# Kernel tuning notes

Hardware: AMD Instinct MI355X
Metric: run time of the kernel (lower is better)

Reference implementation:

```python
import jax, jax.numpy as jnp
import numpy as np

NUM_HEADS = 8
EPS = 1e-6


def setup_inputs() -> dict:
    key = jax.random.key(0)
    ks = jax.random.split(key, 6)
    B, C, H, W = 32, 512, 32, 32
    E = C
    scale = 1.0 / np.sqrt(E)
    x = jax.random.normal(ks[0], (B, C, H, W), dtype=jnp.float32)
    Wq = jax.random.normal(ks[1], (E, E), dtype=jnp.float32) * scale
    Wk = jax.random.normal(ks[2], (E, E), dtype=jnp.float32) * scale
    Wv = jax.random.normal(ks[3], (E, E), dtype=jnp.float32) * scale
    Wo = jax.random.normal(ks[4], (E, E), dtype=jnp.float32) * scale
    bo = jnp.zeros((E,), dtype=jnp.float32)
    return {"x": x, "Wq": Wq, "Wk": Wk, "Wv": Wv, "Wo": Wo, "bo": bo}


def reference(x, Wq, Wk, Wv, Wo, bo):
    B, C, H, W = x.shape
    S = H * W
    nh = NUM_HEADS
    hd = C // nh
    # (B, C, H, W) -> (B, S, C)
    t = x.reshape(B, C, S).transpose(0, 2, 1)
    # torch Linear: t @ W.T  (no bias for q/k/v)
    Q = (t @ Wq.T).reshape(B, S, nh, hd).transpose(0, 2, 1, 3)  # (B, nh, S, hd)
    K = (t @ Wk.T).reshape(B, S, nh, hd).transpose(0, 2, 1, 3)
    V = (t @ Wv.T).reshape(B, S, nh, hd).transpose(0, 2, 1, 3)
    phi_Q = jax.nn.elu(Q) + 1.0
    phi_K = jax.nn.elu(K) + 1.0
    # K^T V aggregation: (B, nh, hd, hd)
    KV = jnp.einsum('bhsd,bhse->bhde', phi_K, V)
    numerator = jnp.einsum('bhsd,bhde->bhse', phi_Q, KV)      # (B, nh, S, hd)
    # phi_K^T @ ones == sum over seq: (B, nh, hd)
    k_sum = jnp.sum(phi_K, axis=2)
    denominator = jnp.einsum('bhsd,bhd->bhs', phi_Q, k_sum)[..., None]  # (B, nh, S, 1)
    out = numerator / (denominator + EPS)
    out = out.transpose(0, 2, 1, 3).reshape(B, S, C)          # (B, S, C)
    out = out @ Wo.T + bo
    out = out.transpose(0, 2, 1).reshape(B, C, H, W)
    return out
```

## Files before the change

### kernel.cpp

```cpp
#include <hip/hip_runtime.h>
#include <hip/hip_bf16.h>

typedef __bf16 bf16;
typedef __bf16 bf16x2 __attribute__((ext_vector_type(2)));
typedef __bf16 bf16x4 __attribute__((ext_vector_type(4)));
typedef __bf16 bf16x8 __attribute__((ext_vector_type(8)));
typedef float  f32x4  __attribute__((ext_vector_type(4)));

#define MFMA16(a,b,c) __builtin_amdgcn_mfma_f32_16x16x32_bf16((a),(b),(c),0,0,0)

constexpr int Cn = 512;
constexpr int Sn = 1024;

__global__ __launch_bounds__(256) void k_cvt_w(const float* __restrict__ Wq,
                                               const float* __restrict__ Wk,
                                               const float* __restrict__ Wv,
                                               const float* __restrict__ Wo,
                                               bf16* __restrict__ Wb) {
    int tid = blockIdx.x * 256 + threadIdx.x;
    int oidx = tid * 8;
    int m  = oidx >> 18;
    int r  = oidx & 262143;
    int gr = r >> 13;
    int kc = (r >> 9) & 15;
    int l  = (r >> 3) & 63;
    const float* s = (m == 0) ? Wq : (m == 1) ? Wk : (m == 2) ? Wv : Wo;
    const float* src = s + (gr * 16 + (l & 15)) * 512 + kc * 32 + (l >> 4) * 8;
    float4 u = ((const float4*)src)[0], v = ((const float4*)src)[1];
    bf16x8 o;
    o[0] = (bf16)u.x; o[1] = (bf16)u.y; o[2] = (bf16)u.z; o[3] = (bf16)u.w;
    o[4] = (bf16)v.x; o[5] = (bf16)v.y; o[6] = (bf16)v.z; o[7] = (bf16)v.w;
    *(bf16x8*)(Wb + oidx) = o;
}

__global__ __launch_bounds__(1024, 4) void k_qkv(const float* __restrict__ x,
                                                 const bf16* __restrict__ Wb,
                                                 bf16* __restrict__ phiQ,
                                                 bf16* __restrict__ kvP,
                                                 float* __restrict__ ksP) {
    int bid = blockIdx.x;
    int st8 = bid & 7, b = bid >> 3;
    int t = threadIdx.x, lane = t & 63, w = t >> 6;
    int l15 = lane & 15, g = lane >> 4;
    int hq   = w >> 2;
    int quad = w & 3;

    __shared__ bf16 xT[64][520];
    __shared__ bf16 pk[4][64][72];
    __shared__ bf16 vv[4][64][72];
    __shared__ float ksl[512];

    if (t < 512) ksl[t] = 0.f;

    int rp = t >> 2;
    int sq = t & 3;

#pragma unroll 1
    for (int sub = 0; sub < 2; ++sub) {
        int srow0 = st8 * 128 + sub * 64;
        {
            const float* xr = x + ((size_t)b * Cn + 2 * rp) * Sn + srow0 + sq * 16;
            float4 f0[4], f1[4];
#pragma unroll
            for (int j = 0; j < 4; ++j) {
                f0[j] = ((const float4*)xr)[j];
                f1[j] = ((const float4*)(xr + Sn))[j];
            }
#pragma unroll
            for (int j = 0; j < 4; ++j) {
                const float* e0 = (const float*)&f0[j];
                const float* e1 = (const float*)&f1[j];
#pragma unroll
                for (int e = 0; e < 4; ++e) {
                    int s = sq * 16 + j * 4 + e;
                    bf16x2 pr;
                    pr[0] = (bf16)e0[e];
                    pr[1] = (bf16)e1[e];
                    *(bf16x2*)&xT[s][2 * rp] = pr;
                }
            }
        }
        __syncthreads();

#pragma unroll 1
        for (int rnd = 0; rnd < 2; ++rnd) {
            int h = rnd * 4 + hq;
            int gr = h * 4 + quad;
            f32x4 aQ[4], aK[4], aV[4];
#pragma unroll
            for (int n = 0; n < 4; ++n) {
                aQ[n] = (f32x4){0.f,0.f,0.f,0.f};
                aK[n] = (f32x4){0.f,0.f,0.f,0.f};
                aV[n] = (f32x4){0.f,0.f,0.f,0.f};
            }
            const bf16* wfQ = Wb + ((size_t)(gr) * 16) * 512 + lane * 8;
            const bf16* wfK = wfQ + (size_t)32 * 16 * 512;
            const bf16* wfV = wfQ + (size_t)64 * 16 * 512;
#pragma unroll 2
            for (int kc = 0; kc < 16; ++kc) {
                bf16x8 fq = *(const bf16x8*)(wfQ + kc * 512);
                bf16x8 fk = *(const bf16x8*)(wfK + kc * 512);
                bf16x8 fv = *(const bf16x8*)(wfV + kc * 512);
#pragma unroll
                for (int n = 0; n < 4; ++n) {
                    bf16x8 bf_ = *(const bf16x8*)&xT[n * 16 + l15][kc * 32 + g * 8];
                    aQ[n] = MFMA16(fq, bf_, aQ[n]);
                    aK[n] = MFMA16(fk, bf_, aK[n]);
                    aV[n] = MFMA16(fv, bf_, aV[n]);
                }
            }
            float kspart[4] = {0.f, 0.f, 0.f, 0.f};
#pragma unroll
            for (int n = 0; n < 4; ++n) {
                bf16x4 qv;
#pragma unroll
                for (int r = 0; r < 4; ++r) {
                    float kv_ = aK[n][r];
                    kv_ = kv_ > 0.f ? kv_ + 1.f : __expf(kv_);
                    bf16 kb = (bf16)kv_;
                    kspart[r] += (float)kb;
                    pk[hq][quad * 16 + g * 4 + r][n * 16 + l15] = kb;
                    vv[hq][quad * 16 + g * 4 + r][n * 16 + l15] = (bf16)aV[n][r];
                    float q = aQ[n][r];
                    q = q > 0.f ? q + 1.f : __expf(q);
                    qv[r] = (bf16)q;
                }
                *(bf16x4*)(phiQ + ((size_t)b * Sn + srow0 + n * 16 + l15) * Cn
                           + h * 64 + quad * 16 + g * 4) = qv;
            }
#pragma unroll
            for (int r = 0; r < 4; ++r) {
                float v = kspart[r];
                v += __shfl_xor(v, 1);
                v += __shfl_xor(v, 2);
                v += __shfl_xor(v, 4);
                v += __shfl_xor(v, 8);
                if (l15 == 0) ksl[h * 64 + quad * 16 + g * 4 + r] += v;
            }
            __syncthreads();
            f32x4 kvacc[4];
#pragma unroll
            for (int n = 0; n < 4; ++n) kvacc[n] = (f32x4){0.f,0.f,0.f,0.f};
#pragma unroll
            for (int k2 = 0; k2 < 2; ++k2) {
                bf16x8 af = *(const bf16x8*)&pk[hq][quad * 16 + l15][k2 * 32 + g * 8];
#pragma unroll
                for (int n = 0; n < 4; ++n) {
                    bf16x8 bf_ = *(const bf16x8*)&vv[hq][n * 16 + l15][k2 * 32 + g * 8];
                    kvacc[n] = MFMA16(af, bf_, kvacc[n]);
                }
            }
            {
                bf16x8 p0, p1;
#pragma unroll
                for (int r = 0; r < 4; ++r) {
                    p0[r]     = (bf16)kvacc[0][r];
                    p0[4 + r] = (bf16)kvacc[1][r];
                    p1[r]     = (bf16)kvacc[2][r];
                    p1[4 + r] = (bf16)kvacc[3][r];
                }
                size_t base = ((size_t)((b * 8 + h) * 16 + st8 * 2 + sub)) * 4096;
                bf16* dst = kvP + base + (size_t)(quad * 64 + lane) * 16;
                *(bf16x8*)(dst)     = p0;
                *(bf16x8*)(dst + 8) = p1;
            }
            __syncthreads();
        }
    }
    if (t < 512) {
        int h = t >> 6, d = t & 63;
        ksP[((b * 8 + h) * 8 + st8) * 64 + d] = ksl[t];
    }
}

__global__ __launch_bounds__(256) void k_red(const bf16* __restrict__ kvP,
                                             const float* __restrict__ ksP,
                                             bf16* __restrict__ KVT,
                                             float* __restrict__ ksum) {
    int bh = blockIdx.x;
    int t = threadIdx.x;
    int wq = t >> 6, lane = t & 63, g = lane >> 4, l15 = lane & 15;
    float acc[16];
#pragma unroll
    for (int i = 0; i < 16; ++i) acc[i] = 0.f;
#pragma unroll
    for (int p = 0; p < 16; ++p) {
        const bf16* src = kvP + ((size_t)bh * 16 + p) * 4096 + (size_t)t * 16;
        bf16x8 v0 = *(const bf16x8*)(src);
        bf16x8 v1 = *(const bf16x8*)(src + 8);
#pragma unroll
        for (int i = 0; i < 8; ++i) { acc[i] += (float)v0[i]; acc[8 + i] += (float)v1[i]; }
    }
#pragma unroll
    for (int n = 0; n < 4; ++n) {
        bf16x4 o;
#pragma unroll
        for (int r = 0; r < 4; ++r) o[r] = (bf16)acc[n * 4 + r];
        *(bf16x4*)(KVT + (size_t)bh * 4096 + (n * 16 + l15) * 64 + wq * 16 + g * 4) = o;
    }
    if (t < 64) {
        float s = 0.f;
#pragma unroll
        for (int p = 0; p < 8; ++p) s += ksP[((size_t)bh * 8 + p) * 64 + t];
        ksum[bh * 64 + t] = s;
    }
}

__global__ __launch_bounds__(1024, 4) void k_apply(const bf16* __restrict__ phiQ,
                                                   const bf16* __restrict__ Wb,
                                                   const bf16* __restrict__ KVT,
                                                   const float* __restrict__ ksum,
                                                   const float* __restrict__ bo,
                                                   float* __restrict__ out) {
    int bid = blockIdx.x;
    int st8 = bid & 7, b = bid >> 3;
    int t = threadIdx.x, lane = t & 63, w = t >> 6, l15 = lane & 15, g = lane >> 4;

    __shared__ bf16 pq[64][520];
    __shared__ float ksl[512];
    __shared__ float rden[64][8];
    __shared__ float bol[512];

    if (t < 512) {
        ksl[t] = ksum[b * 512 + t];
        bol[t] = bo[t];
    }

#pragma unroll 1
    for (int sub = 0; sub < 2; ++sub) {
        int srow0 = st8 * 128 + sub * 64;
        {
            int sr = t >> 4, c0 = (t & 15) * 32;
            const bf16* src = phiQ + ((size_t)b * Sn + srow0 + sr) * Cn + c0;
#pragma unroll
            for (int j = 0; j < 4; ++j)
                *(bf16x8*)&pq[sr][c0 + j * 8] = *(const bf16x8*)(src + j * 8);
        }
        __syncthreads();
        {
            int j = t >> 1, half = t & 1;
            int s = j & 63, h = j >> 6;
            float acc = 0.f;
#pragma unroll
            for (int dt = 0; dt < 4; ++dt) {
                bf16x8 v = *(const bf16x8*)&pq[s][h * 64 + half * 32 + dt * 8];
#pragma unroll
                for (int i = 0; i < 8; ++i)
                    acc += ksl[h * 64 + half * 32 + dt * 8 + i] * (float)v[i];
            }
            acc += __shfl_xor(acc, 1);
            if (half == 0) rden[s][h] = 1.f / (acc + 1e-6f);
        }
        __syncthreads();
        int h = w >> 1, eh = w & 1;
        f32x4 accN[2][4];
#pragma unroll
        for (int mi = 0; mi < 2; ++mi)
#pragma unroll
            for (int n = 0; n < 4; ++n) accN[mi][n] = (f32x4){0.f,0.f,0.f,0.f};
        {
            const bf16* kvb = KVT + ((size_t)(b * 8 + h)) * 4096;
#pragma unroll
            for (int k2 = 0; k2 < 2; ++k2) {
#pragma unroll
                for (int mi = 0; mi < 2; ++mi) {
                    bf16x8 af = *(const bf16x8*)(kvb + (eh * 32 + mi * 16 + l15) * 64 + k2 * 32 + g * 8);
#pragma unroll
                    for (int n = 0; n < 4; ++n) {
                        bf16x8 bf_ = *(const bf16x8*)&pq[n * 16 + l15][h * 64 + k2 * 32 + g * 8];
                        accN[mi][n] = MFMA16(af, bf_, accN[mi][n]);
                    }
                }
            }
        }
        __syncthreads();
#pragma unroll
        for (int mi = 0; mi < 2; ++mi)
#pragma unroll
            for (int n = 0; n < 4; ++n) {
                float rd = rden[n * 16 + l15][h];
                bf16x4 ov;
#pragma unroll
                for (int r = 0; r < 4; ++r) ov[r] = (bf16)(accN[mi][n][r] * rd);
                *(bf16x4*)&pq[n * 16 + l15][h * 64 + eh * 32 + mi * 16 + g * 4] = ov;
            }
        __syncthreads();
        int m0 = w * 32;
        f32x4 acc[2][4];
#pragma unroll
        for (int mi = 0; mi < 2; ++mi)
#pragma unroll
            for (int n = 0; n < 4; ++n) acc[mi][n] = (f32x4){0.f,0.f,0.f,0.f};
        const bf16* WoF = Wb + 786432 + (size_t)(w * 2) * 16 * 512 + lane * 8;
#pragma unroll 2
        for (int kc = 0; kc < 16; ++kc) {
            bf16x8 fa0 = *(const bf16x8*)(WoF + kc * 512);
            bf16x8 fa1 = *(const bf16x8*)(WoF + (16 + kc) * 512);
#pragma unroll
            for (int n = 0; n < 4; ++n) {
                bf16x8 bf_ = *(const bf16x8*)&pq[n * 16 + l15][kc * 32 + g * 8];
                acc[0][n] = MFMA16(fa0, bf_, acc[0][n]);
                acc[1][n] = MFMA16(fa1, bf_, acc[1][n]);
            }
        }
#pragma unroll
        for (int mi = 0; mi < 2; ++mi)
#pragma unroll
            for (int r = 0; r < 4; ++r) {
                int co = m0 + mi * 16 + g * 4 + r;
                float bb = bol[co];
#pragma unroll
                for (int n = 0; n < 4; ++n)
                    out[((size_t)b * Cn + co) * Sn + srow0 + n * 16 + l15] = acc[mi][n][r] + bb;
            }
        __syncthreads();
    }
}

extern "C" void kernel_launch(void* const* d_in, const int* in_sizes, int n_in,
                              void* d_out, int out_size, void* d_ws, size_t ws_size,
                              hipStream_t stream) {
    const float* x  = (const float*)d_in[0];
    const float* Wq = (const float*)d_in[1];
    const float* Wk = (const float*)d_in[2];
    const float* Wv = (const float*)d_in[3];
    const float* Wo = (const float*)d_in[4];
    const float* bo = (const float*)d_in[5];
    float* out = (float*)d_out;

    char* ws = (char*)d_ws;
    bf16*  phiQ = (bf16*)ws;
    bf16*  Wb   = (bf16*)(ws + 33554432);
    float* ksP  = (float*)(ws + 35651584);
    bf16*  KVT  = (bf16*)(ws + 36175872);
    float* ks   = (float*)(ws + 38273024);

    bf16*  kvP  = (bf16*)d_out;

    k_cvt_w <<< 512,  256, 0, stream>>>(Wq, Wk, Wv, Wo, Wb);
    k_qkv   <<< 256, 1024, 0, stream>>>(x, Wb, phiQ, kvP, ksP);
    k_red   <<< 256,  256, 0, stream>>>(kvP, ksP, KVT, ks);
    k_apply <<< 256, 1024, 0, stream>>>(phiQ, Wb, KVT, ks, bo, out);
}
```

Before: 119.7 us.

## Prefetch second x sub-tile into registers and overlap with projection compute

The global load of the second 64-row x sub-tile is issued at kernel start and held in registers, then converted and written to LDS after the last projection round of the first sub-tile. This hides global load latency behind MFMA work and removes one block-wide barrier per sub-tile. __syncthreads is replaced with a custom barrier that only waits on LDS counters, so outstanding global stores and loads do not stall the barrier. The cost is higher register pressure from the held prefetch data, and the barrier relies on xT not being read during the KV phase.

```diff
diff --git a/kernel.cpp b/kernel.cpp
--- a/kernel.cpp
+++ b/kernel.cpp
@@ -11,6 +11,12 @@
 
 constexpr int Cn = 512;
 constexpr int Sn = 1024;
+
+__device__ __forceinline__ void bar_lds() {
+    asm volatile("s_waitcnt lgkmcnt(0)" ::: "memory");
+    __builtin_amdgcn_sched_barrier(0);
+    __builtin_amdgcn_s_barrier();
+}
 
 __global__ __launch_bounds__(256) void k_cvt_w(const float* __restrict__ Wq,
                                                const float* __restrict__ Wk,
@@ -53,35 +59,38 @@
     if (t < 512) ksl[t] = 0.f;
 
     int rp = t >> 2;
-    int sq = t & 3;
+    int sq = (t & 3) << 4;
+
+    const float* xr0 = x + ((size_t)b * Cn + 2 * rp) * Sn + st8 * 128 + sq;
+    {
+        float4 f0[4], f1[4];
+#pragma unroll
+        for (int j = 0; j < 4; ++j) {
+            f0[j] = ((const float4*)xr0)[j];
+            f1[j] = ((const float4*)(xr0 + Sn))[j];
+        }
+#pragma unroll
+        for (int j = 0; j < 4; ++j) {
+            const float* e0 = (const float*)&f0[j];
+            const float* e1 = (const float*)&f1[j];
+#pragma unroll
+            for (int e = 0; e < 4; ++e) {
+                bf16x2 pr; pr[0] = (bf16)e0[e]; pr[1] = (bf16)e1[e];
+                *(bf16x2*)&xT[sq + j * 4 + e][2 * rp] = pr;
+            }
+        }
+    }
+    float4 fB0[4], fB1[4];
+#pragma unroll
+    for (int j = 0; j < 4; ++j) {
+        fB0[j] = ((const float4*)(xr0 + 64))[j];
+        fB1[j] = ((const float4*)(xr0 + 64 + Sn))[j];
+    }
+    __syncthreads();
 
 #pragma unroll 1
     for (int sub = 0; sub < 2; ++sub) {
         int srow0 = st8 * 128 + sub * 64;
-        {
-            const float* xr = x + ((size_t)b * Cn + 2 * rp) * Sn + srow0 + sq * 16;
-            float4 f0[4], f1[4];
-#pragma unroll
-            for (int j = 0; j < 4; ++j) {
-                f0[j] = ((const float4*)xr)[j];
-                f1[j] = ((const float4*)(xr + Sn))[j];
-            }
-#pragma unroll
-            for (int j = 0; j < 4; ++j) {
-                const float* e0 = (const float*)&f0[j];
-                const float* e1 = (const float*)&f1[j];
-#pragma unroll
-                for (int e = 0; e < 4; ++e) {
-                    int s = sq * 16 + j * 4 + e;
-                    bf16x2 pr;
-                    pr[0] = (bf16)e0[e];
-                    pr[1] = (bf16)e1[e];
-                    *(bf16x2*)&xT[s][2 * rp] = pr;
-                }
-            }
-        }
-        __syncthreads();
-
 #pragma unroll 1
         for (int rnd = 0; rnd < 2; ++rnd) {
             int h = rnd * 4 + hq;
@@ -93,7 +102,7 @@
                 aK[n] = (f32x4){0.f,0.f,0.f,0.f};
                 aV[n] = (f32x4){0.f,0.f,0.f,0.f};
             }
-            const bf16* wfQ = Wb + ((size_t)(gr) * 16) * 512 + lane * 8;
+            const bf16* wfQ = Wb + ((size_t)gr * 16) * 512 + lane * 8;
             const bf16* wfK = wfQ + (size_t)32 * 16 * 512;
             const bf16* wfV = wfQ + (size_t)64 * 16 * 512;
 #pragma unroll 2
@@ -137,7 +146,19 @@
                 v += __shfl_xor(v, 8);
                 if (l15 == 0) ksl[h * 64 + quad * 16 + g * 4 + r] += v;
             }
-            __syncthreads();
+            bar_lds();
+            if (sub == 0 && rnd == 1) {
+#pragma unroll
+                for (int j = 0; j < 4; ++j) {
+                    const float* e0 = (const float*)&fB0[j];
+                    const float* e1 = (const float*)&fB1[j];
+#pragma unroll
+                    for (int e = 0; e < 4; ++e) {
+                        bf16x2 pr; pr[0] = (bf16)e0[e]; pr[1] = (bf16)e1[e];
+                        *(bf16x2*)&xT[sq + j * 4 + e][2 * rp] = pr;
+                    }
+                }
+            }
             f32x4 kvacc[4];
 #pragma unroll
             for (int n = 0; n < 4; ++n) kvacc[n] = (f32x4){0.f,0.f,0.f,0.f};
@@ -164,7 +185,7 @@
                 *(bf16x8*)(dst)     = p0;
                 *(bf16x8*)(dst + 8) = p1;
             }
-            __syncthreads();
+            bar_lds();
         }
     }
     if (t < 512) {
```

Measured after the change: 116.0 us. -3.1%, faster.
